# Performance work log

Hardware: AMD Instinct MI355X
Metric: run time of the kernel (lower is better)

Reference implementation:

```python
import jax, jax.numpy as jnp
import numpy as np

NUM_EXPERTS = 8
TOP_K = 2
DIM = 1024
HIDDEN = 4096
B, S = 4, 2048


def setup_inputs() -> dict:
    key = jax.random.key(0)
    ks = jax.random.split(key, 6)
    scale = 0.02
    x = jax.random.normal(ks[0], (B, S, DIM), dtype=jnp.float32)
    wg = jax.random.normal(ks[1], (NUM_EXPERTS, DIM), dtype=jnp.float32) * scale
    bg = jnp.zeros((NUM_EXPERTS,), dtype=jnp.float32)
    Wgate = jax.random.normal(ks[2], (NUM_EXPERTS, HIDDEN, DIM), dtype=jnp.float32) * scale
    Wup = jax.random.normal(ks[3], (NUM_EXPERTS, HIDDEN, DIM), dtype=jnp.float32) * scale
    Wdown = jax.random.normal(ks[4], (NUM_EXPERTS, DIM, HIDDEN), dtype=jnp.float32) * scale
    return {"x": x, "wg": wg, "bg": bg, "Wgate": Wgate, "Wup": Wup, "Wdown": Wdown}


def reference(x, wg, bg, Wgate, Wup, Wdown):
    b, s, d = x.shape
    xf = x.reshape(-1, d)  # [T, D]
    T = xf.shape[0]
    # --- gating: top-k over router logits, softmax over masked logits ---
    logits = xf @ wg.T + bg  # [T, E]
    vals, idx = jax.lax.top_k(logits, TOP_K)  # [T, K]
    masked = jnp.full_like(logits, -jnp.inf)
    rows = jnp.arange(T)[:, None]
    masked = masked.at[rows, idx].set(vals)
    weights = jax.nn.softmax(masked, axis=-1)  # zeros outside top-k
    # --- experts: weighted SwiGLU sum (weight is 0 for non-routed tokens,
    # so this matches the gather/scatter loop exactly) ---
    out = jnp.zeros_like(xf)
    for e in range(NUM_EXPERTS):
        g = xf @ Wgate[e].T            # [T, H]
        u = xf @ Wup[e].T              # [T, H]
        h = (g * jax.nn.sigmoid(g)) * u
        out = out + (h @ Wdown[e].T) * weights[:, e:e + 1]
    return out.reshape(b, s, d)
```

## Files before the change

### kernel.cpp

```cpp
#include <hip/hip_runtime.h>
#include <cstdint>
#include <cstddef>

typedef unsigned short ushort_t;
typedef __attribute__((ext_vector_type(8))) __bf16 bf16x8;
typedef __attribute__((ext_vector_type(8))) short  s16x8;
typedef __attribute__((ext_vector_type(4))) float  f32x4;

#define NE 8
#define DIM 1024
#define HIDDEN 4096
#define NTOK 8192
#define CAP NTOK
#define NROWS (NTOK * 2)

#define BM 128
#define BN 64
#define BK 32
#define LDP 40

static constexpr size_t WS_COUNTS  = 0;
static constexpr size_t WS_OFFSETS = 256;
static constexpr size_t WS_TOKENS  = 512;
static constexpr size_t WS_WEIGHTS = WS_TOKENS + (size_t)NE * CAP * 4;
static constexpr size_t WS_H       = ((WS_WEIGHTS + (size_t)NE * CAP * 4 + 1023) / 1024) * 1024;

__device__ __forceinline__ ushort_t cvt_bf16(float f) {
  unsigned u = __float_as_uint(f);
  return (ushort_t)((u + 0x7FFFu + ((u >> 16) & 1u)) >> 16);
}

__device__ __forceinline__ void st8(ushort_t* dst, float4 a, float4 b) {
  s16x8 v;
  v[0] = (short)cvt_bf16(a.x); v[1] = (short)cvt_bf16(a.y);
  v[2] = (short)cvt_bf16(a.z); v[3] = (short)cvt_bf16(a.w);
  v[4] = (short)cvt_bf16(b.x); v[5] = (short)cvt_bf16(b.y);
  v[6] = (short)cvt_bf16(b.z); v[7] = (short)cvt_bf16(b.w);
  *reinterpret_cast<s16x8*>(dst) = v;
}

__device__ __forceinline__ bf16x8 ldb(const ushort_t* p) {
  union { s16x8 s; bf16x8 b; } u;
  u.s = *reinterpret_cast<const s16x8*>(p);
  return u.b;
}

__device__ __forceinline__ f32x4 mfma16(bf16x8 a, bf16x8 b, f32x4 c) {
  return __builtin_amdgcn_mfma_f32_16x16x32_bf16(a, b, c, 0, 0, 0);
}

__global__ __launch_bounds__(256) void gating_kernel(
    const float* __restrict__ x, const float* __restrict__ wg,
    const float* __restrict__ bg, int* __restrict__ counts,
    int* __restrict__ token_list, float* __restrict__ weight_list) {
  int gid  = blockIdx.x * blockDim.x + threadIdx.x;
  int tok  = gid >> 6;
  int lane = threadIdx.x & 63;
  if (tok >= NTOK) return;
  const float* xr = x + (size_t)tok * DIM;

  float part[NE];
#pragma unroll
  for (int e = 0; e < NE; ++e) part[e] = 0.f;
  for (int i = lane; i < DIM; i += 64) {
    float xv = xr[i];
#pragma unroll
    for (int e = 0; e < NE; ++e) part[e] = fmaf(xv, wg[e * DIM + i], part[e]);
  }
#pragma unroll
  for (int e = 0; e < NE; ++e) {
    float v = part[e];
#pragma unroll
    for (int o = 32; o > 0; o >>= 1) v += __shfl_xor(v, o, 64);
    part[e] = v + bg[e];
  }
  if (lane == 0) {
    int i0 = 0; float v0 = part[0];
#pragma unroll
    for (int e = 1; e < NE; ++e) if (part[e] > v0) { v0 = part[e]; i0 = e; }
    int i1 = -1; float v1 = -INFINITY;
#pragma unroll
    for (int e = 0; e < NE; ++e) if (e != i0 && part[e] > v1) { v1 = part[e]; i1 = e; }
    float e1 = expf(v1 - v0);
    float s  = 1.f + e1;
    float w0 = 1.f / s;
    float w1 = e1 / s;
    int s0 = atomicAdd(&counts[i0], 1);
    token_list[i0 * CAP + s0]  = tok;
    weight_list[i0 * CAP + s0] = w0;
    int s1 = atomicAdd(&counts[i1], 1);
    token_list[i1 * CAP + s1]  = tok;
    weight_list[i1 * CAP + s1] = w1;
  }
}

__global__ void prefix_kernel(const int* __restrict__ counts, int* __restrict__ offsets) {
  if (threadIdx.x == 0) {
    int acc = 0;
    for (int e = 0; e < NE; ++e) { offsets[e] = acc; acc += counts[e]; }
  }
}

__global__ __launch_bounds__(256) void stage1_kernel(
    const float* __restrict__ x, const float* __restrict__ Wgate,
    const float* __restrict__ Wup, const int* __restrict__ counts,
    const int* __restrict__ offsets, const int* __restrict__ token_list,
    ushort_t* __restrict__ h) {
  const int e  = blockIdx.z;
  const int mt = blockIdx.y;
  const int nt = blockIdx.x;
  const int count = counts[e];
  if (mt * BM >= count) return;

  __shared__ __align__(16) ushort_t Xs[BM][LDP];
  __shared__ __align__(16) ushort_t Gs[BN][LDP];
  __shared__ __align__(16) ushort_t Us[BN][LDP];
  __shared__ int toks[BM];

  const int t = threadIdx.x;
  if (t < BM) {
    int m = mt * BM + t;
    toks[t] = token_list[e * CAP + (m < count ? m : count - 1)];
  }
  __syncthreads();

  const float* Wg = Wgate + (size_t)e * HIDDEN * DIM + (size_t)(nt * BN) * DIM;
  const float* Wu = Wup   + (size_t)e * HIDDEN * DIM + (size_t)(nt * BN) * DIM;

  const int wid  = t >> 6;
  const int lane = t & 63;
  const int wm   = wid & 1;
  const int wn   = wid >> 1;
  const int fr   = lane & 15;
  const int kg   = lane >> 4;

  f32x4 accg[4][2], accu[4][2];
#pragma unroll
  for (int i = 0; i < 4; ++i)
#pragma unroll
    for (int j = 0; j < 2; ++j) { accg[i][j] = (f32x4)0.f; accu[i][j] = (f32x4)0.f; }

  const int sr = t >> 2;
  const int sc = (t & 3) * 8;

  const int tok0 = toks[sr];
  const int tok1 = toks[sr + 64];
  const float* xp0 = x + (size_t)tok0 * DIM + sc;
  const float* xp1 = x + (size_t)tok1 * DIM + sc;
  const float* gp  = Wg + (size_t)sr * DIM + sc;
  const float* up  = Wu + (size_t)sr * DIM + sc;

  for (int k0 = 0; k0 < DIM; k0 += BK) {
    float4 a0 = *reinterpret_cast<const float4*>(xp0 + k0);
    float4 a1 = *reinterpret_cast<const float4*>(xp0 + k0 + 4);
    float4 b0 = *reinterpret_cast<const float4*>(xp1 + k0);
    float4 b1 = *reinterpret_cast<const float4*>(xp1 + k0 + 4);
    float4 g0 = *reinterpret_cast<const float4*>(gp + k0);
    float4 g1 = *reinterpret_cast<const float4*>(gp + k0 + 4);
    float4 u0 = *reinterpret_cast<const float4*>(up + k0);
    float4 u1 = *reinterpret_cast<const float4*>(up + k0 + 4);
    st8(&Xs[sr][sc],      a0, a1);
    st8(&Xs[sr + 64][sc], b0, b1);
    st8(&Gs[sr][sc],      g0, g1);
    st8(&Us[sr][sc],      u0, u1);
    __syncthreads();

    bf16x8 bg0 = ldb(&Gs[wn * 32 + fr][kg * 8]);
    bf16x8 bg1 = ldb(&Gs[wn * 32 + 16 + fr][kg * 8]);
    bf16x8 bu0 = ldb(&Us[wn * 32 + fr][kg * 8]);
    bf16x8 bu1 = ldb(&Us[wn * 32 + 16 + fr][kg * 8]);
#pragma unroll
    for (int mf = 0; mf < 4; ++mf) {
      bf16x8 a = ldb(&Xs[wm * 64 + mf * 16 + fr][kg * 8]);
      accg[mf][0] = mfma16(a, bg0, accg[mf][0]);
      accg[mf][1] = mfma16(a, bg1, accg[mf][1]);
      accu[mf][0] = mfma16(a, bu0, accu[mf][0]);
      accu[mf][1] = mfma16(a, bu1, accu[mf][1]);
    }
    __syncthreads();
  }

  const size_t slot0 = (size_t)offsets[e];
  const int nbase = nt * BN + wn * 32;
#pragma unroll
  for (int mf = 0; mf < 4; ++mf) {
#pragma unroll
    for (int r = 0; r < 4; ++r) {
      int ml = wm * 64 + mf * 16 + kg * 4 + r;
      int m  = mt * BM + ml;
      if (m < count) {
        size_t rowoff = (slot0 + m) * (size_t)HIDDEN + nbase;
#pragma unroll
        for (int nf = 0; nf < 2; ++nf) {
          float g  = accg[mf][nf][r];
          float uu = accu[mf][nf][r];
          float hv = g / (1.f + __expf(-g)) * uu;
          h[rowoff + nf * 16 + fr] = cvt_bf16(hv);
        }
      }
    }
  }
}

__global__ __launch_bounds__(256) void stage2_kernel(
    const ushort_t* __restrict__ h, const float* __restrict__ Wdown,
    const int* __restrict__ counts, const int* __restrict__ offsets,
    const int* __restrict__ token_list, const float* __restrict__ weight_list,
    float* __restrict__ out) {
  const int e  = blockIdx.z;
  const int mt = blockIdx.y;
  const int nt = blockIdx.x;
  const int count = counts[e];
  if (mt * BM >= count) return;

  __shared__ __align__(16) ushort_t As[BM][LDP];
  __shared__ __align__(16) ushort_t Ds[BN][LDP];
  __shared__ int   toks[BM];
  __shared__ float wts[BM];

  const int t = threadIdx.x;
  if (t < BM) {
    int m  = mt * BM + t;
    int mc = m < count ? m : count - 1;
    toks[t] = token_list[e * CAP + mc];
    wts[t]  = weight_list[e * CAP + mc];
  }
  __syncthreads();

  const float* Wd = Wdown + (size_t)e * DIM * HIDDEN + (size_t)(nt * BN) * HIDDEN;
  const int slot0b = offsets[e] + mt * BM;

  const int wid  = t >> 6;
  const int lane = t & 63;
  const int wm   = wid & 1;
  const int wn   = wid >> 1;
  const int fr   = lane & 15;
  const int kg   = lane >> 4;

  f32x4 acc[4][2];
#pragma unroll
  for (int i = 0; i < 4; ++i)
#pragma unroll
    for (int j = 0; j < 2; ++j) acc[i][j] = (f32x4)0.f;

  const int sr = t >> 2;
  const int sc = (t & 3) * 8;

  int r0 = slot0b + sr;       r0 = r0 < NROWS ? r0 : NROWS - 1;
  int r1 = slot0b + sr + 64;  r1 = r1 < NROWS ? r1 : NROWS - 1;
  const ushort_t* hp0 = h + (size_t)r0 * HIDDEN + sc;
  const ushort_t* hp1 = h + (size_t)r1 * HIDDEN + sc;
  const float*    dp  = Wd + (size_t)sr * HIDDEN + sc;

  for (int k0 = 0; k0 < HIDDEN; k0 += BK) {
    s16x8 ha = *reinterpret_cast<const s16x8*>(hp0 + k0);
    s16x8 hb = *reinterpret_cast<const s16x8*>(hp1 + k0);
    float4 d0 = *reinterpret_cast<const float4*>(dp + k0);
    float4 d1 = *reinterpret_cast<const float4*>(dp + k0 + 4);
    *reinterpret_cast<s16x8*>(&As[sr][sc])      = ha;
    *reinterpret_cast<s16x8*>(&As[sr + 64][sc]) = hb;
    st8(&Ds[sr][sc], d0, d1);
    __syncthreads();

    bf16x8 b0 = ldb(&Ds[wn * 32 + fr][kg * 8]);
    bf16x8 b1 = ldb(&Ds[wn * 32 + 16 + fr][kg * 8]);
#pragma unroll
    for (int mf = 0; mf < 4; ++mf) {
      bf16x8 a = ldb(&As[wm * 64 + mf * 16 + fr][kg * 8]);
      acc[mf][0] = mfma16(a, b0, acc[mf][0]);
      acc[mf][1] = mfma16(a, b1, acc[mf][1]);
    }
    __syncthreads();
  }

  const int nbase = nt * BN + wn * 32;
#pragma unroll
  for (int mf = 0; mf < 4; ++mf) {
#pragma unroll
    for (int r = 0; r < 4; ++r) {
      int ml = wm * 64 + mf * 16 + kg * 4 + r;
      int m  = mt * BM + ml;
      if (m < count) {
        int   tok = toks[ml];
        float w   = wts[ml];
        size_t o  = (size_t)tok * DIM + nbase;
#pragma unroll
        for (int nf = 0; nf < 2; ++nf) {
          atomicAdd(&out[o + nf * 16 + fr], acc[mf][nf][r] * w);
        }
      }
    }
  }
}

extern "C" void kernel_launch(void* const* d_in, const int* in_sizes, int n_in,
                              void* d_out, int out_size, void* d_ws, size_t ws_size,
                              hipStream_t stream) {
  const float* x     = (const float*)d_in[0];
  const float* wg    = (const float*)d_in[1];
  const float* bg    = (const float*)d_in[2];
  const float* Wgate = (const float*)d_in[3];
  const float* Wup   = (const float*)d_in[4];
  const float* Wdown = (const float*)d_in[5];
  float* out = (float*)d_out;

  char* ws = (char*)d_ws;
  int*      counts      = (int*)(ws + WS_COUNTS);
  int*      offsets     = (int*)(ws + WS_OFFSETS);
  int*      token_list  = (int*)(ws + WS_TOKENS);
  float*    weight_list = (float*)(ws + WS_WEIGHTS);
  ushort_t* h           = (ushort_t*)(ws + WS_H);

  hipMemsetAsync(counts, 0, NE * sizeof(int), stream);
  hipMemsetAsync(out, 0, (size_t)NTOK * DIM * sizeof(float), stream);

  gating_kernel<<<NTOK / 4, 256, 0, stream>>>(x, wg, bg, counts, token_list, weight_list);
  prefix_kernel<<<1, 64, 0, stream>>>(counts, offsets);
  stage1_kernel<<<dim3(HIDDEN / BN, CAP / BM, NE), 256, 0, stream>>>(
      x, Wgate, Wup, counts, offsets, token_list, h);
  stage2_kernel<<<dim3(DIM / BN, CAP / BM, NE), 256, 0, stream>>>(
      h, Wdown, counts, offsets, token_list, weight_list, out);
}
```

Measured before the change: 1.382 ms.

## Pre-convert inputs and weights to bf16 and stream tiles via global_load_lds

```diff
diff --git a/kernel.cpp b/kernel.cpp
--- a/kernel.cpp
+++ b/kernel.cpp
@@ -24,6 +24,15 @@
 static constexpr size_t WS_TOKENS  = 512;
 static constexpr size_t WS_WEIGHTS = WS_TOKENS + (size_t)NE * CAP * 4;
 static constexpr size_t WS_H       = ((WS_WEIGHTS + (size_t)NE * CAP * 4 + 1023) / 1024) * 1024;
+static constexpr size_t H_BYTES    = (size_t)NROWS * HIDDEN * 2;
+static constexpr size_t WS_XB      = WS_H + H_BYTES;
+static constexpr size_t XB_BYTES   = (size_t)NTOK * DIM * 2;
+static constexpr size_t W_BYTES    = (size_t)NE * HIDDEN * DIM * 2;
+static constexpr size_t WS_WGB     = WS_XB + XB_BYTES;
+static constexpr size_t WS_WUB     = WS_WGB + W_BYTES;
+static constexpr size_t WS_WDB     = WS_WUB + W_BYTES;
+static constexpr size_t WS_T1_END  = WS_WDB;
+static constexpr size_t WS_T2_END  = WS_WDB + W_BYTES;
 
 __device__ __forceinline__ ushort_t cvt_bf16(float f) {
   unsigned u = __float_as_uint(f);
@@ -45,8 +54,29 @@
   return u.b;
 }
 
+__device__ __forceinline__ bf16x8 ldt(const ushort_t* base, int row, int s) {
+  return ldb(base + (size_t)((row << 2) + (s ^ ((row >> 1) & 3))) * 8);
+}
+
 __device__ __forceinline__ f32x4 mfma16(bf16x8 a, bf16x8 b, f32x4 c) {
   return __builtin_amdgcn_mfma_f32_16x16x32_bf16(a, b, c, 0, 0, 0);
+}
+
+#define GLDS16(g, l)                                                     \
+  __builtin_amdgcn_global_load_lds(                                      \
+      (const __attribute__((address_space(1))) unsigned int*)(g),        \
+      (__attribute__((address_space(3))) unsigned int*)(l), 16, 0, 0)
+
+__global__ __launch_bounds__(256) void cvt_kernel(const float* __restrict__ s,
+                                                  ushort_t* __restrict__ d, long n8) {
+  long i = (long)blockIdx.x * 256 + threadIdx.x;
+  long stride = (long)gridDim.x * 256;
+  for (long p = i; p < n8; p += stride) {
+    const float4* sp = reinterpret_cast<const float4*>(s) + 2 * p;
+    float4 a = sp[0];
+    float4 b = sp[1];
+    st8(d + p * 8, a, b);
+  }
 }
 
 __global__ __launch_bounds__(256) void gating_kernel(
@@ -102,6 +132,198 @@
 }
 
 __global__ __launch_bounds__(256) void stage1_kernel(
+    const ushort_t* __restrict__ xb, const ushort_t* __restrict__ wgb,
+    const ushort_t* __restrict__ wub, const int* __restrict__ counts,
+    const int* __restrict__ offsets, const int* __restrict__ token_list,
+    ushort_t* __restrict__ h) {
+  const int e  = blockIdx.z;
+  const int mt = blockIdx.y;
+  const int nt = blockIdx.x;
+  const int count = counts[e];
+  if (mt * BM >= count) return;
+
+  __shared__ __align__(16) ushort_t XsL[BM * 32];
+  __shared__ __align__(16) ushort_t GsL[BN * 32];
+  __shared__ __align__(16) ushort_t UsL[BN * 32];
+  __shared__ int toks[BM];
+
+  const int t = threadIdx.x;
+  if (t < BM) {
+    int m = mt * BM + t;
+    toks[t] = token_list[e * CAP + (m < count ? m : count - 1)];
+  }
+  __syncthreads();
+
+  const int wid  = t >> 6;
+  const int lane = t & 63;
+  const int wm   = wid & 1;
+  const int wn   = wid >> 1;
+  const int fr   = lane & 15;
+  const int kg   = lane >> 4;
+
+  const int uA = wid * 128 + lane;
+  const int uB = uA + 64;
+  const int rA = uA >> 2, sA = (uA & 3) ^ ((rA >> 1) & 3);
+  const int rB = uB >> 2, sB = (uB & 3) ^ ((rB >> 1) & 3);
+  const ushort_t* gxA = xb + (size_t)toks[rA] * DIM + sA * 8;
+  const ushort_t* gxB = xb + (size_t)toks[rB] * DIM + sB * 8;
+
+  const int uG = wid * 64 + lane;
+  const int rG = uG >> 2, sG = (uG & 3) ^ ((rG >> 1) & 3);
+  const size_t wrow = (size_t)e * HIDDEN + (size_t)nt * BN + rG;
+  const ushort_t* ggp = wgb + wrow * DIM + sG * 8;
+  const ushort_t* gup = wub + wrow * DIM + sG * 8;
+
+  ushort_t* ldsXA = XsL + (size_t)(wid * 128) * 8;
+  ushort_t* ldsXB = XsL + (size_t)(wid * 128 + 64) * 8;
+  ushort_t* ldsG  = GsL + (size_t)(wid * 64) * 8;
+  ushort_t* ldsU  = UsL + (size_t)(wid * 64) * 8;
+
+  f32x4 accg[4][2], accu[4][2];
+#pragma unroll
+  for (int i = 0; i < 4; ++i)
+#pragma unroll
+    for (int j = 0; j < 2; ++j) { accg[i][j] = (f32x4)0.f; accu[i][j] = (f32x4)0.f; }
+
+  for (int k0 = 0; k0 < DIM; k0 += BK) {
+    GLDS16(gxA + k0, ldsXA);
+    GLDS16(gxB + k0, ldsXB);
+    GLDS16(ggp + k0, ldsG);
+    GLDS16(gup + k0, ldsU);
+    __syncthreads();
+
+    bf16x8 bg0 = ldt(GsL, wn * 32 + fr, kg);
+    bf16x8 bg1 = ldt(GsL, wn * 32 + 16 + fr, kg);
+    bf16x8 bu0 = ldt(UsL, wn * 32 + fr, kg);
+    bf16x8 bu1 = ldt(UsL, wn * 32 + 16 + fr, kg);
+#pragma unroll
+    for (int mf = 0; mf < 4; ++mf) {
+      bf16x8 a = ldt(XsL, wm * 64 + mf * 16 + fr, kg);
+      accg[mf][0] = mfma16(a, bg0, accg[mf][0]);
+      accg[mf][1] = mfma16(a, bg1, accg[mf][1]);
+      accu[mf][0] = mfma16(a, bu0, accu[mf][0]);
+      accu[mf][1] = mfma16(a, bu1, accu[mf][1]);
+    }
+    __syncthreads();
+  }
+
+  const size_t slot0 = (size_t)offsets[e];
+  const int nbase = nt * BN + wn * 32;
+#pragma unroll
+  for (int mf = 0; mf < 4; ++mf) {
+#pragma unroll
+    for (int r = 0; r < 4; ++r) {
+      int ml = wm * 64 + mf * 16 + kg * 4 + r;
+      int m  = mt * BM + ml;
+      if (m < count) {
+        size_t rowoff = (slot0 + m) * (size_t)HIDDEN + nbase;
+#pragma unroll
+        for (int nf = 0; nf < 2; ++nf) {
+          float g  = accg[mf][nf][r];
+          float uu = accu[mf][nf][r];
+          float hv = g / (1.f + __expf(-g)) * uu;
+          h[rowoff + nf * 16 + fr] = cvt_bf16(hv);
+        }
+      }
+    }
+  }
+}
+
+__global__ __launch_bounds__(256) void stage2_kernel(
+    const ushort_t* __restrict__ h, const ushort_t* __restrict__ wdb,
+    const int* __restrict__ counts, const int* __restrict__ offsets,
+    const int* __restrict__ token_list, const float* __restrict__ weight_list,
+    float* __restrict__ out) {
+  const int e  = blockIdx.z;
+  const int mt = blockIdx.y;
+  const int nt = blockIdx.x;
+  const int count = counts[e];
+  if (mt * BM >= count) return;
+
+  __shared__ __align__(16) ushort_t AsL[BM * 32];
+  __shared__ __align__(16) ushort_t DsL[BN * 32];
+  __shared__ int   toks[BM];
+  __shared__ float wts[BM];
+
+  const int t = threadIdx.x;
+  if (t < BM) {
+    int m  = mt * BM + t;
+    int mc = m < count ? m : count - 1;
+    toks[t] = token_list[e * CAP + mc];
+    wts[t]  = weight_list[e * CAP + mc];
+  }
+  __syncthreads();
+
+  const int wid  = t >> 6;
+  const int lane = t & 63;
+  const int wm   = wid & 1;
+  const int wn   = wid >> 1;
+  const int fr   = lane & 15;
+  const int kg   = lane >> 4;
+
+  const int slot0b = offsets[e] + mt * BM;
+
+  const int uA = wid * 128 + lane;
+  const int uB = uA + 64;
+  const int rA = uA >> 2, sA = (uA & 3) ^ ((rA >> 1) & 3);
+  const int rB = uB >> 2, sB = (uB & 3) ^ ((rB >> 1) & 3);
+  int hrA = slot0b + rA; hrA = hrA < NROWS ? hrA : NROWS - 1;
+  int hrB = slot0b + rB; hrB = hrB < NROWS ? hrB : NROWS - 1;
+  const ushort_t* ghA = h + (size_t)hrA * HIDDEN + sA * 8;
+  const ushort_t* ghB = h + (size_t)hrB * HIDDEN + sB * 8;
+
+  const int uD = wid * 64 + lane;
+  const int rD = uD >> 2, sD = (uD & 3) ^ ((rD >> 1) & 3);
+  const ushort_t* gdp = wdb + ((size_t)e * DIM + (size_t)nt * BN + rD) * HIDDEN + sD * 8;
+
+  ushort_t* ldsAA = AsL + (size_t)(wid * 128) * 8;
+  ushort_t* ldsAB = AsL + (size_t)(wid * 128 + 64) * 8;
+  ushort_t* ldsD  = DsL + (size_t)(wid * 64) * 8;
+
+  f32x4 acc[4][2];
+#pragma unroll
+  for (int i = 0; i < 4; ++i)
+#pragma unroll
+    for (int j = 0; j < 2; ++j) acc[i][j] = (f32x4)0.f;
+
+  for (int k0 = 0; k0 < HIDDEN; k0 += BK) {
+    GLDS16(ghA + k0, ldsAA);
+    GLDS16(ghB + k0, ldsAB);
+    GLDS16(gdp + k0, ldsD);
+    __syncthreads();
+
+    bf16x8 b0 = ldt(DsL, wn * 32 + fr, kg);
+    bf16x8 b1 = ldt(DsL, wn * 32 + 16 + fr, kg);
+#pragma unroll
+    for (int mf = 0; mf < 4; ++mf) {
+      bf16x8 a = ldt(AsL, wm * 64 + mf * 16 + fr, kg);
+      acc[mf][0] = mfma16(a, b0, acc[mf][0]);
+      acc[mf][1] = mfma16(a, b1, acc[mf][1]);
+    }
+    __syncthreads();
+  }
+
+  const int nbase = nt * BN + wn * 32;
+#pragma unroll
+  for (int mf = 0; mf < 4; ++mf) {
+#pragma unroll
+    for (int r = 0; r < 4; ++r) {
+      int ml = wm * 64 + mf * 16 + kg * 4 + r;
+      int m  = mt * BM + ml;
+      if (m < count) {
+        int   tok = toks[ml];
+        float w   = wts[ml];
+        size_t o  = (size_t)tok * DIM + nbase;
+#pragma unroll
+        for (int nf = 0; nf < 2; ++nf) {
+          atomicAdd(&out[o + nf * 16 + fr], acc[mf][nf][r] * w);
+        }
+      }
+    }
+  }
+}
+
+__global__ __launch_bounds__(256) void stage1_f32w(
     const float* __restrict__ x, const float* __restrict__ Wgate,
     const float* __restrict__ Wup, const int* __restrict__ counts,
     const int* __restrict__ offsets, const int* __restrict__ token_list,
@@ -202,7 +424,7 @@
   }
 }
 
-__global__ __launch_bounds__(256) void stage2_kernel(
+__global__ __launch_bounds__(256) void stage2_f32w(
     const ushort_t* __restrict__ h, const float* __restrict__ Wdown,
     const int* __restrict__ counts, const int* __restrict__ offsets,
     const int* __restrict__ token_list, const float* __restrict__ weight_list,
@@ -316,8 +538,37 @@
 
   gating_kernel<<<NTOK / 4, 256, 0, stream>>>(x, wg, bg, counts, token_list, weight_list);
   prefix_kernel<<<1, 64, 0, stream>>>(counts, offsets);
-  stage1_kernel<<<dim3(HIDDEN / BN, CAP / BM, NE), 256, 0, stream>>>(
-      x, Wgate, Wup, counts, offsets, token_list, h);
-  stage2_kernel<<<dim3(DIM / BN, CAP / BM, NE), 256, 0, stream>>>(
-      h, Wdown, counts, offsets, token_list, weight_list, out);
-}
+
+  const bool tier1 = ws_size >= WS_T1_END;
+  const bool tier2 = ws_size >= WS_T2_END;
+
+  if (tier1) {
+    ushort_t* xb  = (ushort_t*)(ws + WS_XB);
+    ushort_t* wgb = (ushort_t*)(ws + WS_WGB);
+    ushort_t* wub = (ushort_t*)(ws + WS_WUB);
+
+    long w8 = (long)NE * HIDDEN * DIM / 8;
+    long x8 = (long)NTOK * DIM / 8;
+    cvt_kernel<<<8192, 256, 0, stream>>>(Wgate, wgb, w8);
+    cvt_kernel<<<8192, 256, 0, stream>>>(Wup,   wub, w8);
+    cvt_kernel<<<4096, 256, 0, stream>>>(x,     xb,  x8);
+
+    stage1_kernel<<<dim3(HIDDEN / BN, CAP / BM, NE), 256, 0, stream>>>(
+        xb, wgb, wub, counts, offsets, token_list, h);
+
+    if (tier2) {
+      ushort_t* wdb = (ushort_t*)(ws + WS_WDB);
+      cvt_kernel<<<8192, 256, 0, stream>>>(Wdown, wdb, w8);
+      stage2_kernel<<<dim3(DIM / BN, CAP / BM, NE), 256, 0, stream>>>(
+          h, wdb, counts, offsets, token_list, weight_list, out);
+    } else {
+      stage2_f32w<<<dim3(DIM / BN, CAP / BM, NE), 256, 0, stream>>>(
+          h, Wdown, counts, offsets, token_list, weight_list, out);
+    }
+  } else {
+    stage1_f32w<<<dim3(HIDDEN / BN, CAP / BM, NE), 256, 0, stream>>>(
+        x, Wgate, Wup, counts, offsets, token_list, h);
+    stage2_f32w<<<dim3(DIM / BN, CAP / BM, NE), 256, 0, stream>>>(
+        h, Wdown, counts, offsets, token_list, weight_list, out);
+  }
+}
```

After: 1.246 ms. 1.11x faster.
